# Optimization experiments

Hardware: AMD Instinct MI355X
Metric: run time of the kernel (lower is better)

The kernel has to match this reference:

```python
import jax, jax.numpy as jnp
import numpy as np

N_CB = 10          # n_codebooks
K = 2048           # codebook_size
D = 256            # codebook_dim
SEM = 256          # semantic_proj_dim
W2V = 1024         # w2v_bert_dim
COMMIT = 0.25      # commitment_cost


def setup_inputs() -> dict:
    key = jax.random.key(0)
    ks = jax.random.split(key, 7)
    B, T = 16, 1024
    z = jax.random.normal(ks[0], (B, T, D), jnp.float32)
    w2v_targets = jax.random.normal(ks[1], (B, T, W2V), jnp.float32)
    # codebooks: uniform(-1/K, 1/K) as in nn.init.uniform_
    E = jax.random.uniform(ks[2], (N_CB, K, D), jnp.float32, -1.0 / K, 1.0 / K)
    # semantic head: Linear(D, SEM) -> GELU -> Linear(SEM, W2V)
    W1 = jax.random.normal(ks[3], (D, SEM), jnp.float32) * (1.0 / np.sqrt(D))
    b1 = jnp.zeros((SEM,), jnp.float32)
    W2 = jax.random.normal(ks[4], (SEM, W2V), jnp.float32) * (1.0 / np.sqrt(SEM))
    b2 = jnp.zeros((W2V,), jnp.float32)
    return {"z": z, "w2v_targets": w2v_targets, "E": E,
            "W1": W1, "b1": b1, "W2": W2, "b2": b2}


def _vq_step(residual, Ei):
    """Single-codebook VQ with straight-through estimator.
    residual: (B,T,D); Ei: (K,D). Returns (z_q, indices, loss)."""
    sg = jax.lax.stop_gradient
    B, T, d = residual.shape
    flat = residual.reshape(-1, d)                      # (N, D)
    dist = (jnp.sum(flat * flat, axis=1, keepdims=True)
            - 2.0 * flat @ Ei.T
            + jnp.sum(Ei * Ei, axis=1))
    idx = jnp.argmin(dist, axis=1).reshape(B, T)        # (B, T)
    q = Ei[idx]                                         # (B, T, D) gather
    commitment_loss = jnp.mean((sg(q) - residual) ** 2)
    embedding_loss = jnp.mean((q - sg(residual)) ** 2)
    loss = embedding_loss + COMMIT * commitment_loss
    z_q = residual + sg(q - residual)                   # straight-through
    return z_q, idx, loss


def reference(z, w2v_targets, E, W1, b1, W2, b2):
    residual = z
    z_q_total = jnp.zeros_like(z)
    codes = []
    vq_loss = jnp.float32(0.0)
    semantic_loss = jnp.float32(0.0)
    for i in range(N_CB):
        z_q_i, idx_i, loss_i = _vq_step(residual, E[i])
        if i == 0:
            # semantic head on CB1 output (torch GELU default = exact erf)
            h = jax.nn.gelu(z_q_i @ W1 + b1, approximate=False)
            predicted = h @ W2 + b2                     # (B, T, W2V)
            semantic_loss = jnp.mean((predicted - w2v_targets) ** 2)
        z_q_total = z_q_total + z_q_i
        residual = residual - jax.lax.stop_gradient(z_q_i)
        vq_loss = vq_loss + loss_i
        codes.append(idx_i)
    all_codes = jnp.stack(codes, axis=-1)               # (B, T, N_CB)
    return z_q_total, all_codes, vq_loss, semantic_loss
```

## Files before the change

kernel.cpp:

```cpp
#include <hip/hip_runtime.h>
#include <float.h>
#include <math.h>

#define NTOK 16384
#define KCB  2048
#define DDIM 256
#define NCB  10
#define MARGIN 1.0e-3f

typedef __attribute__((ext_vector_type(8))) short  short8;
typedef __attribute__((ext_vector_type(4))) float  f32x4;

static __device__ __forceinline__ unsigned short f2bf(float f) {
    unsigned int b = __float_as_uint(f);
    unsigned int r = b + 0x7FFFu + ((b >> 16) & 1u);
    return (unsigned short)(r >> 16);
}
static __device__ __forceinline__ float bf2f(unsigned short h) {
    return __uint_as_float((unsigned int)h << 16);
}

__global__ __launch_bounds__(256) void norms_all_kernel(const float* __restrict__ E,
                                                        const float* __restrict__ z,
                                                        float* __restrict__ sseE,
                                                        float* __restrict__ normA) {
    const int gw   = (blockIdx.x * 256 + threadIdx.x) >> 6;
    const int lane = threadIdx.x & 63;
    const int row  = gw * 4 + (lane >> 4);
    const int l    = lane & 15;
    const float* src = nullptr; float* dst = nullptr;
    if (row < NCB * KCB)             { src = E + (size_t)row * DDIM;               dst = sseE + row; }
    else if (row < NCB * KCB + NTOK) { src = z + (size_t)(row - NCB * KCB) * DDIM; dst = normA + (row - NCB * KCB); }
    float r = 0.f;
    if (src) {
        const float* a = src + ((l >> 3) << 7) + (l & 7);
        float v = a[0];
        r = __fmul_rn(v, v);
        #pragma unroll
        for (int k = 1; k < 16; ++k) { v = a[k * 8]; r = __fadd_rn(r, __fmul_rn(v, v)); }
    }
    r = __fadd_rn(r, __shfl_xor(r, 1, 64));
    r = __fadd_rn(r, __shfl_xor(r, 2, 64));
    r = __fadd_rn(r, __shfl_xor(r, 4, 64));
    r = __fadd_rn(r, __shfl_xor(r, 8, 64));
    if (src && l == 0) *dst = r;
}

__global__ __launch_bounds__(256) void conv_all_kernel(const float* __restrict__ E,
                                                       const float* __restrict__ z,
                                                       const float* __restrict__ W1,
                                                       const float* __restrict__ W2,
                                                       unsigned short* __restrict__ Eh,
                                                       unsigned short* __restrict__ resH,
                                                       unsigned short* __restrict__ w1t,
                                                       unsigned short* __restrict__ w2t) {
    int i = blockIdx.x * 256 + threadIdx.x;
    if (i < 5242880) {
        Eh[i] = f2bf(E[i]);
    } else if (i < 9437184) {
        int j = i - 5242880;
        resH[j] = f2bf(z[j]);
    } else if (i < 9502720) {
        int j = i - 9437184;
        int n = j >> 8, k = j & 255;
        w1t[j] = f2bf(W1[k * 256 + n]);
    } else {
        int j = i - 9502720;
        int n = j >> 8, k = j & 255;
        w2t[j] = f2bf(W2[k * 1024 + n]);
    }
}

__global__ __launch_bounds__(256) void vq_screen(const unsigned short* __restrict__ resH,
                                                 const unsigned short* __restrict__ Ehi,
                                                 const float* __restrict__ sseEi,
                                                 int2* __restrict__ gSlots,
                                                 int* __restrict__ gCnt,
                                                 float* __restrict__ gMin) {
    __shared__ unsigned short sAh[128 * 40];
    __shared__ unsigned short sBh[128 * 40];
    __shared__ float sC[128];
    __shared__ int   lCnt[128];
    __shared__ int2  lSlot[128][4];
    const int tid = threadIdx.x;
    const int wv = tid >> 6, lane = tid & 63;
    const int l15 = lane & 15, qd = lane >> 4;
    const int tile = blockIdx.x >> 4, slice = blockIdx.x & 15;
    const int t0 = tile * 128, c0 = slice * 128;

    if (tid < 128) { lCnt[tid] = 0; sC[tid] = sseEi[c0 + tid]; }
    {
        int2 inf; inf.x = 0x7F800000; inf.y = 0;
        ((int2*)lSlot)[tid] = inf; ((int2*)lSlot)[tid + 256] = inf;
    }

    f32x4 acc[2][8];
    #pragma unroll
    for (int m = 0; m < 2; ++m)
        #pragma unroll
        for (int n = 0; n < 8; ++n) acc[m][n] = (f32x4){0.f, 0.f, 0.f, 0.f};

    const int r0 = tid >> 2, cc4 = tid & 3;
    const int r1 = (tid + 256) >> 2;
    for (int kc = 0; kc < 8; ++kc) {
        const int db = kc * 32;
        __syncthreads();
        *(uint4*)(sAh + r0 * 40 + cc4 * 8) = *(const uint4*)(resH + (size_t)(t0 + r0) * 256 + db + cc4 * 8);
        *(uint4*)(sAh + r1 * 40 + cc4 * 8) = *(const uint4*)(resH + (size_t)(t0 + r1) * 256 + db + cc4 * 8);
        *(uint4*)(sBh + r0 * 40 + cc4 * 8) = *(const uint4*)(Ehi  + (size_t)(c0 + r0) * 256 + db + cc4 * 8);
        *(uint4*)(sBh + r1 * 40 + cc4 * 8) = *(const uint4*)(Ehi  + (size_t)(c0 + r1) * 256 + db + cc4 * 8);
        __syncthreads();

        short8 ah[2];
        #pragma unroll
        for (int m = 0; m < 2; ++m)
            ah[m] = *(const short8*)(sAh + (wv * 32 + m * 16 + l15) * 40 + qd * 8);
        #pragma unroll
        for (int n = 0; n < 8; ++n) {
            short8 bh = *(const short8*)(sBh + (n * 16 + l15) * 40 + qd * 8);
            #pragma unroll
            for (int m = 0; m < 2; ++m)
                acc[m][n] = __builtin_amdgcn_mfma_f32_16x16x32_bf16(ah[m], bh, acc[m][n], 0, 0, 0);
        }
    }

    #pragma unroll
    for (int m = 0; m < 2; ++m)
        #pragma unroll
        for (int n = 0; n < 8; ++n) {
            float Cv = sC[n * 16 + l15];
            #pragma unroll
            for (int r = 0; r < 4; ++r) acc[m][n][r] = fmaf(-2.f, acc[m][n][r], Cv);
        }
    #pragma unroll
    for (int m = 0; m < 2; ++m)
        #pragma unroll
        for (int r = 0; r < 4; ++r) {
            float v = acc[m][0][r];
            #pragma unroll
            for (int n = 1; n < 8; ++n) v = fminf(v, acc[m][n][r]);
            v = fminf(v, __shfl_xor(v, 1, 64));
            v = fminf(v, __shfl_xor(v, 2, 64));
            v = fminf(v, __shfl_xor(v, 4, 64));
            v = fminf(v, __shfl_xor(v, 8, 64));
            int tloc = wv * 32 + m * 16 + qd * 4 + r;
            if (l15 == 0) gMin[(t0 + tloc) * 16 + slice] = v;
            float thr = v + MARGIN;
            #pragma unroll
            for (int n = 0; n < 8; ++n) {
                float sv = acc[m][n][r];
                if (sv <= thr) {
                    int pos = atomicAdd(&lCnt[tloc], 1);
                    if (pos < 4) {
                        int2 e; e.x = __float_as_int(sv); e.y = c0 + n * 16 + l15;
                        lSlot[tloc][pos] = e;
                    }
                }
            }
        }
    __syncthreads();
    {
        int tloc = tid >> 1, half = tid & 1;
        size_t base = (size_t)(t0 + tloc) * 64 + slice * 4 + half * 2;
        gSlots[base]     = lSlot[tloc][half * 2];
        gSlots[base + 1] = lSlot[tloc][half * 2 + 1];
        if (!half) gCnt[(t0 + tloc) * 16 + slice] = lCnt[tloc];
    }
}

static __device__ __forceinline__ float np_chain(const float* __restrict__ sRow,
                                                 const float* __restrict__ Ei,
                                                 int cc, float A, float C) {
    const float4* e = (const float4*)(Ei + (size_t)cc * DDIM);
    float a = 0.f;
    #pragma unroll 8
    for (int k = 0; k < 64; ++k) {
        float4 ev = e[k];
        const float4 rv = *(const float4*)(sRow + k * 4);
        a = fmaf(rv.x, ev.x, a); a = fmaf(rv.y, ev.y, a);
        a = fmaf(rv.z, ev.z, a); a = fmaf(rv.w, ev.w, a);
    }
    return __fadd_rn(fmaf(-2.f, a, A), C);
}

__global__ __launch_bounds__(256) void vq_post(const float* __restrict__ resSrc,
                                               const float* __restrict__ Ei,
                                               const float* __restrict__ sseEi,
                                               float* __restrict__ res,
                                               float* __restrict__ zq,
                                               float* __restrict__ codes,
                                               float* __restrict__ lossPart,
                                               float* __restrict__ normA,
                                               unsigned short* __restrict__ resHp,
                                               unsigned short* __restrict__ zqb,
                                               const int2* __restrict__ gSlots,
                                               const int* __restrict__ gCnt,
                                               const float* __restrict__ gMin,
                                               int iter) {
    __shared__ float sScr[4][4][256];
    const int tid = threadIdx.x;
    const int wv = tid >> 6, lane = tid & 63;
    const int g = lane >> 4, l15 = lane & 15;
    const int tb = blockIdx.x * 16 + wv * 4;
    float lsum = 0.f;

    int2 sl[4]; float4 r4[4]; int cnt4[4]; float smin4[4]; float4 zq4[4]; float A4[4];
    #pragma unroll
    for (int j = 0; j < 4; ++j) sl[j] = gSlots[(size_t)(tb + j) * 64 + lane];
    #pragma unroll
    for (int j = 0; j < 4; ++j)
        r4[j] = *(const float4*)(resSrc + (size_t)(tb + j) * DDIM + lane * 4);
    #pragma unroll
    for (int j = 0; j < 4; ++j) cnt4[j]  = (lane < 16) ? gCnt[(tb + j) * 16 + lane] : 0;
    #pragma unroll
    for (int j = 0; j < 4; ++j) smin4[j] = (lane < 16) ? gMin[(tb + j) * 16 + lane] : FLT_MAX;
    #pragma unroll
    for (int j = 0; j < 4; ++j) A4[j] = normA[tb + j];
    if (iter > 0) {
        #pragma unroll
        for (int j = 0; j < 4; ++j)
            zq4[j] = *(const float4*)(zq + (size_t)(tb + j) * DDIM + lane * 4);
    }

    int winner[4];
    #pragma unroll
    for (int j = 0; j < 4; ++j) {
        float gm = smin4[j];
        #pragma unroll
        for (int o = 32; o >= 1; o >>= 1) gm = fminf(gm, __shfl_xor(gm, o, 64));
        const float thr = gm + MARGIN;
        float sv = __int_as_float(sl[j].x);
        unsigned long long bal = __ballot((sv <= thr) ? 1 : 0);
        bool ovfRel = __any((lane < 16 && cnt4[j] > 4 && smin4[j] <= thr) ? 1 : 0);
        if (!ovfRel && __popcll(bal) == 1) {
            winner[j] = __shfl(sl[j].y, __ffsll(bal) - 1, 64);
        } else if (!ovfRel) {
            *(float4*)(&sScr[wv][j][lane * 4]) = r4[j];
            const bool qal = (sv <= thr);
            const int cc = qal ? sl[j].y : 0;
            float s = np_chain(sScr[wv][j], Ei, cc, A4[j], sseEi[cc]);
            unsigned long long best = qal
                ? (((unsigned long long)__float_as_uint(s) << 32) | (unsigned)cc)
                : ~0ULL;
            #pragma unroll
            for (int o = 32; o >= 1; o >>= 1) {
                unsigned long long ot = __shfl_xor(best, o, 64);
                if (ot < best) best = ot;
            }
            winner[j] = (int)(unsigned)(best & 0xFFFFFFFFu);
        } else {
            *(float4*)(&sScr[wv][j][lane * 4]) = r4[j];
            unsigned long long best = ~0ULL;
            for (int cc = lane; cc < KCB; cc += 64) {
                float s = np_chain(sScr[wv][j], Ei, cc, A4[j], sseEi[cc]);
                unsigned long long key =
                    ((unsigned long long)__float_as_uint(s) << 32) | (unsigned)cc;
                if (key < best) best = key;
            }
            #pragma unroll
            for (int o = 32; o >= 1; o >>= 1) {
                unsigned long long ot = __shfl_xor(best, o, 64);
                if (ot < best) best = ot;
            }
            winner[j] = (int)(unsigned)(best & 0xFFFFFFFFu);
        }
    }
    #pragma unroll
    for (int j = 0; j < 4; ++j)
        if (lane == j) codes[(size_t)(tb + j) * NCB + iter] = (float)winner[j];

    float4 q4[4];
    #pragma unroll
    for (int j = 0; j < 4; ++j)
        q4[j] = *(const float4*)(Ei + (size_t)winner[j] * DDIM + lane * 4);

    #pragma unroll
    for (int j = 0; j < 4; ++j) {
        const size_t go = (size_t)(tb + j) * DDIM + lane * 4;
        float4 rn4, zqi4;
        float tqx = q4[j].x - r4[j].x; zqi4.x = r4[j].x + tqx; rn4.x = r4[j].x - zqi4.x;
        float tqy = q4[j].y - r4[j].y; zqi4.y = r4[j].y + tqy; rn4.y = r4[j].y - zqi4.y;
        float tqz = q4[j].z - r4[j].z; zqi4.z = r4[j].z + tqz; rn4.z = r4[j].z - zqi4.z;
        float tqw = q4[j].w - r4[j].w; zqi4.w = r4[j].w + tqw; rn4.w = r4[j].w - zqi4.w;
        lsum = fmaf(tqx, tqx, lsum); lsum = fmaf(tqy, tqy, lsum);
        lsum = fmaf(tqz, tqz, lsum); lsum = fmaf(tqw, tqw, lsum);
        *(float4*)(res + go) = rn4;
        {
            unsigned short h[4] = { f2bf(rn4.x), f2bf(rn4.y), f2bf(rn4.z), f2bf(rn4.w) };
            *(ushort4*)(resHp + go) = *(ushort4*)h;
        }
        if (iter == 0) {
            *(float4*)(zq + go) = zqi4;
            unsigned short u[4] = { f2bf(zqi4.x), f2bf(zqi4.y), f2bf(zqi4.z), f2bf(zqi4.w) };
            *(ushort4*)(zqb + go) = *(ushort4*)u;
        } else {
            zq4[j].x += zqi4.x; zq4[j].y += zqi4.y;
            zq4[j].z += zqi4.z; zq4[j].w += zqi4.w;
            *(float4*)(zq + go) = zq4[j];
        }
        *(float4*)(&sScr[wv][j][lane * 4]) = rn4;
    }
    {
        const float* a = &sScr[wv][g][((l15 >> 3) << 7) + (l15 & 7)];
        float v = a[0];
        float r = __fmul_rn(v, v);
        #pragma unroll
        for (int k = 1; k < 16; ++k) { v = a[k * 8]; r = __fadd_rn(r, __fmul_rn(v, v)); }
        r = __fadd_rn(r, __shfl_xor(r, 1, 64));
        r = __fadd_rn(r, __shfl_xor(r, 2, 64));
        r = __fadd_rn(r, __shfl_xor(r, 4, 64));
        r = __fadd_rn(r, __shfl_xor(r, 8, 64));
        if (l15 == 0) normA[tb + g] = r;
    }
    #pragma unroll
    for (int o = 32; o >= 1; o >>= 1) lsum += __shfl_xor(lsum, o, 64);
    if (lane == 0) lossPart[iter * 4096 + blockIdx.x * 4 + wv] = lsum;
}

__global__ __launch_bounds__(256) void loss_final(const float* __restrict__ lossPart,
                                                  float* __restrict__ vql) {
    __shared__ float sRed[4];
    float s = 0.f;
    for (int i = threadIdx.x; i < 40960; i += 256) s += lossPart[i];
    #pragma unroll
    for (int o = 32; o >= 1; o >>= 1) s += __shfl_xor(s, o, 64);
    if ((threadIdx.x & 63) == 0) sRed[threadIdx.x >> 6] = s;
    __syncthreads();
    if (threadIdx.x == 0)
        vql[0] = (sRed[0] + sRed[1] + sRed[2] + sRed[3]) * (1.25f / 4194304.f);
}

__global__ __launch_bounds__(256) void semantic_mfma(const unsigned short* __restrict__ zqb,
                                                     const float* __restrict__ tgt,
                                                     const unsigned short* __restrict__ w1t,
                                                     const float* __restrict__ b1,
                                                     const unsigned short* __restrict__ w2t,
                                                     const float* __restrict__ b2,
                                                     float* __restrict__ semLoss) {
    __shared__ unsigned short sZ[32 * 264];
    __shared__ unsigned short sH[32 * 264];
    __shared__ float sRed[4];
    const int tid = threadIdx.x;
    const int wv = tid >> 6, lane = tid & 63;
    const int l15 = lane & 15, qd = lane >> 4;
    const int tb = blockIdx.x * 32;

    {
        int row = tid >> 3, seg = tid & 7;
        const uint4* src = (const uint4*)(zqb + (size_t)(tb + row) * 256);
        uint4* dst = (uint4*)(&sZ[row * 264]);
        #pragma unroll
        for (int p = 0; p < 4; ++p) dst[seg * 4 + p] = src[seg * 4 + p];
    }
    __syncthreads();

    short8 az[8][2];
    #pragma unroll
    for (int kc = 0; kc < 8; ++kc)
        #pragma unroll
        for (int m = 0; m < 2; ++m)
            az[kc][m] = *(const short8*)(&sZ[(16 * m + l15) * 264 + kc * 32 + qd * 8]);

    #pragma unroll
    for (int nt4 = 0; nt4 < 4; ++nt4) {
        const int nt = wv * 4 + nt4;
        f32x4 acc0 = {0.f,0.f,0.f,0.f}, acc1 = {0.f,0.f,0.f,0.f};
        const unsigned short* bb = w1t + (size_t)(16 * nt + l15) * 256 + qd * 8;
        #pragma unroll
        for (int kc = 0; kc < 8; ++kc) {
            short8 b = *(const short8*)(bb + kc * 32);
            acc0 = __builtin_amdgcn_mfma_f32_16x16x32_bf16(az[kc][0], b, acc0, 0, 0, 0);
            acc1 = __builtin_amdgcn_mfma_f32_16x16x32_bf16(az[kc][1], b, acc1, 0, 0, 0);
        }
        const float b1v = b1[16 * nt + l15];
        #pragma unroll
        for (int r = 0; r < 4; ++r) {
            float x0 = acc0[r] + b1v;
            float x1 = acc1[r] + b1v;
            sH[(4 * qd + r) * 264 + 16 * nt + l15]      = f2bf(0.5f * x0 * (1.f + erff(x0 * 0.70710678f)));
            sH[(16 + 4 * qd + r) * 264 + 16 * nt + l15] = f2bf(0.5f * x1 * (1.f + erff(x1 * 0.70710678f)));
        }
    }
    __syncthreads();

    short8 ah[8][2];
    #pragma unroll
    for (int kc = 0; kc < 8; ++kc)
        #pragma unroll
        for (int m = 0; m < 2; ++m)
            ah[kc][m] = *(const short8*)(&sH[(16 * m + l15) * 264 + kc * 32 + qd * 8]);

    float lsum = 0.f;
    for (int t = 0; t < 16; ++t) {
        const int nt = wv * 16 + t;
        f32x4 acc0 = {0.f,0.f,0.f,0.f}, acc1 = {0.f,0.f,0.f,0.f};
        const unsigned short* bb = w2t + (size_t)(16 * nt + l15) * 256 + qd * 8;
        #pragma unroll
        for (int kc = 0; kc < 8; ++kc) {
            short8 b = *(const short8*)(bb + kc * 32);
            acc0 = __builtin_amdgcn_mfma_f32_16x16x32_bf16(ah[kc][0], b, acc0, 0, 0, 0);
            acc1 = __builtin_amdgcn_mfma_f32_16x16x32_bf16(ah[kc][1], b, acc1, 0, 0, 0);
        }
        const int n = 16 * nt + l15;
        const float b2v = b2[n];
        #pragma unroll
        for (int r = 0; r < 4; ++r) {
            float dv0 = (acc0[r] + b2v) - tgt[(size_t)(tb + 4 * qd + r) * 1024 + n];
            float dv1 = (acc1[r] + b2v) - tgt[(size_t)(tb + 16 + 4 * qd + r) * 1024 + n];
            lsum = fmaf(dv0, dv0, lsum);
            lsum = fmaf(dv1, dv1, lsum);
        }
    }
    #pragma unroll
    for (int o = 32; o >= 1; o >>= 1) lsum += __shfl_xor(lsum, o, 64);
    if (lane == 0) sRed[wv] = lsum;
    __syncthreads();
    if (tid == 0)
        atomicAdd(semLoss, (sRed[0] + sRed[1] + sRed[2] + sRed[3]) * (1.0f / 16777216.f));
}

extern "C" void kernel_launch(void* const* d_in, const int* in_sizes, int n_in,
                              void* d_out, int out_size, void* d_ws, size_t ws_size,
                              hipStream_t stream) {
    const float* z   = (const float*)d_in[0];
    const float* tgt = (const float*)d_in[1];
    const float* E   = (const float*)d_in[2];
    const float* W1  = (const float*)d_in[3];
    const float* b1  = (const float*)d_in[4];
    const float* W2  = (const float*)d_in[5];
    const float* b2  = (const float*)d_in[6];

    float* out   = (float*)d_out;
    float* zq    = out;
    float* codes = out + (size_t)NTOK * DDIM;
    float* vql   = codes + (size_t)NTOK * NCB;

    char* w = (char*)d_ws;
    float*          res   = (float*)(w);
    unsigned short* resH  = (unsigned short*)(w + 16777216);
    unsigned short* Eh    = (unsigned short*)(w + 33554432);
    unsigned short* zqb   = (unsigned short*)(w + 54525952);
    int2*           gSlots= (int2*)(w + 62914560);
    int*            gCnt  = (int*)(w + 71303168);
    float*          gMin  = (float*)(w + 72351744);
    float*          sseE  = (float*)(w + 73400320);
    float*          normA = (float*)(w + 73531392);
    float*          lossPart=(float*)(w + 73662464);
    unsigned short* w1t   = (unsigned short*)(w + 73924608);
    unsigned short* w2t   = (unsigned short*)(w + 74055680);

    hipMemsetAsync(vql, 0, 2 * sizeof(float), stream);
    norms_all_kernel<<<9216, 256, 0, stream>>>(E, z, sseE, normA);
    conv_all_kernel<<<38144, 256, 0, stream>>>(E, z, W1, W2, Eh, resH, w1t, w2t);
    for (int it = 0; it < NCB; ++it) {
        const float*          Ei    = E  + (size_t)it * KCB * DDIM;
        const unsigned short* Ehi   = Eh + (size_t)it * KCB * DDIM;
        const float*          sseEi = sseE + (size_t)it * KCB;
        const float* resSrc = (it == 0) ? z : res;
        vq_screen<<<2048, 256, 0, stream>>>(resH, Ehi, sseEi, gSlots, gCnt, gMin);
        vq_post<<<1024, 256, 0, stream>>>(resSrc, Ei, sseEi, res, zq, codes, lossPart,
                                          normA, resH, zqb, gSlots, gCnt, gMin, it);
        if (it == 0)
            semantic_mfma<<<512, 256, 0, stream>>>(zqb, tgt, w1t, b1, w2t, b2, vql + 1);
    }
    loss_final<<<1, 256, 0, stream>>>(lossPart, vql);
}
```

Before: 1.103 ms.

## Fuse semantic head into second screen launch and merge prep kernels

Merges the norms and bf16 conversion kernels into one prep launch. Removes the standalone semantic-head launch and folds its blocks into the iteration-1 screen kernel, interleaving one semantic block per four screen blocks and sharing LDS through a union, so the semantic GEMMs overlap with the codebook screening. It also halves the vq_post block size to 128 threads with twice as many blocks, and prefetches targets in the semantic loop. The costs are a larger LDS footprint for the fused kernel, possible load imbalance between heterogeneous blocks, and scheduling changes from the resized post kernel.

```diff
diff --git a/kernel.cpp b/kernel.cpp
--- a/kernel.cpp
+++ b/kernel.cpp
@@ -20,78 +20,86 @@
     return __uint_as_float((unsigned int)h << 16);
 }
 
-__global__ __launch_bounds__(256) void norms_all_kernel(const float* __restrict__ E,
-                                                        const float* __restrict__ z,
-                                                        float* __restrict__ sseE,
-                                                        float* __restrict__ normA) {
-    const int gw   = (blockIdx.x * 256 + threadIdx.x) >> 6;
-    const int lane = threadIdx.x & 63;
-    const int row  = gw * 4 + (lane >> 4);
-    const int l    = lane & 15;
-    const float* src = nullptr; float* dst = nullptr;
-    if (row < NCB * KCB)             { src = E + (size_t)row * DDIM;               dst = sseE + row; }
-    else if (row < NCB * KCB + NTOK) { src = z + (size_t)(row - NCB * KCB) * DDIM; dst = normA + (row - NCB * KCB); }
-    float r = 0.f;
-    if (src) {
-        const float* a = src + ((l >> 3) << 7) + (l & 7);
-        float v = a[0];
-        r = __fmul_rn(v, v);
-        #pragma unroll
-        for (int k = 1; k < 16; ++k) { v = a[k * 8]; r = __fadd_rn(r, __fmul_rn(v, v)); }
-    }
-    r = __fadd_rn(r, __shfl_xor(r, 1, 64));
-    r = __fadd_rn(r, __shfl_xor(r, 2, 64));
-    r = __fadd_rn(r, __shfl_xor(r, 4, 64));
-    r = __fadd_rn(r, __shfl_xor(r, 8, 64));
-    if (src && l == 0) *dst = r;
-}
-
-__global__ __launch_bounds__(256) void conv_all_kernel(const float* __restrict__ E,
-                                                       const float* __restrict__ z,
-                                                       const float* __restrict__ W1,
-                                                       const float* __restrict__ W2,
-                                                       unsigned short* __restrict__ Eh,
-                                                       unsigned short* __restrict__ resH,
-                                                       unsigned short* __restrict__ w1t,
-                                                       unsigned short* __restrict__ w2t) {
-    int i = blockIdx.x * 256 + threadIdx.x;
-    if (i < 5242880) {
-        Eh[i] = f2bf(E[i]);
-    } else if (i < 9437184) {
-        int j = i - 5242880;
-        resH[j] = f2bf(z[j]);
-    } else if (i < 9502720) {
-        int j = i - 9437184;
-        int n = j >> 8, k = j & 255;
-        w1t[j] = f2bf(W1[k * 256 + n]);
+__global__ __launch_bounds__(256) void prep_all(const float* __restrict__ E,
+                                                const float* __restrict__ z,
+                                                const float* __restrict__ W1,
+                                                const float* __restrict__ W2,
+                                                float* __restrict__ sseE,
+                                                float* __restrict__ normA,
+                                                unsigned short* __restrict__ Eh,
+                                                unsigned short* __restrict__ resH,
+                                                unsigned short* __restrict__ w1t,
+                                                unsigned short* __restrict__ w2t) {
+    if (blockIdx.x < 38144) {
+        int i = blockIdx.x * 256 + threadIdx.x;
+        if (i < 5242880) {
+            Eh[i] = f2bf(E[i]);
+        } else if (i < 9437184) {
+            int j = i - 5242880;
+            resH[j] = f2bf(z[j]);
+        } else if (i < 9502720) {
+            int j = i - 9437184;
+            int n = j >> 8, k = j & 255;
+            w1t[j] = f2bf(W1[k * 256 + n]);
+        } else {
+            int j = i - 9502720;
+            int n = j >> 8, k = j & 255;
+            w2t[j] = f2bf(W2[k * 1024 + n]);
+        }
     } else {
-        int j = i - 9502720;
-        int n = j >> 8, k = j & 255;
-        w2t[j] = f2bf(W2[k * 1024 + n]);
-    }
-}
-
-__global__ __launch_bounds__(256) void vq_screen(const unsigned short* __restrict__ resH,
-                                                 const unsigned short* __restrict__ Ehi,
-                                                 const float* __restrict__ sseEi,
-                                                 int2* __restrict__ gSlots,
-                                                 int* __restrict__ gCnt,
-                                                 float* __restrict__ gMin) {
-    __shared__ unsigned short sAh[128 * 40];
-    __shared__ unsigned short sBh[128 * 40];
-    __shared__ float sC[128];
-    __shared__ int   lCnt[128];
-    __shared__ int2  lSlot[128][4];
+        const int gw   = ((blockIdx.x - 38144) * 256 + threadIdx.x) >> 6;
+        const int lane = threadIdx.x & 63;
+        const int row  = gw * 4 + (lane >> 4);
+        const int l    = lane & 15;
+        const float* src = nullptr; float* dst = nullptr;
+        if (row < NCB * KCB)             { src = E + (size_t)row * DDIM;               dst = sseE + row; }
+        else if (row < NCB * KCB + NTOK) { src = z + (size_t)(row - NCB * KCB) * DDIM; dst = normA + (row - NCB * KCB); }
+        float r = 0.f;
+        if (src) {
+            const float* a = src + ((l >> 3) << 7) + (l & 7);
+            float v = a[0];
+            r = __fmul_rn(v, v);
+            #pragma unroll
+            for (int k = 1; k < 16; ++k) { v = a[k * 8]; r = __fadd_rn(r, __fmul_rn(v, v)); }
+        }
+        r = __fadd_rn(r, __shfl_xor(r, 1, 64));
+        r = __fadd_rn(r, __shfl_xor(r, 2, 64));
+        r = __fadd_rn(r, __shfl_xor(r, 4, 64));
+        r = __fadd_rn(r, __shfl_xor(r, 8, 64));
+        if (src && l == 0) *dst = r;
+    }
+}
+
+struct ScrLds {
+    unsigned short sAh[128 * 40];
+    unsigned short sBh[128 * 40];
+    float sC[128];
+    int   lCnt[128];
+    int2  lSlot[128][4];
+};
+struct SemLds {
+    unsigned short sZ[32 * 264];
+    float sRed[4];
+};
+union FusedLds { ScrLds scr; SemLds sem; };
+
+static __device__ __forceinline__ void screen_body(const int scrIdx, ScrLds& L,
+                                                   const unsigned short* __restrict__ resH,
+                                                   const unsigned short* __restrict__ Ehi,
+                                                   const float* __restrict__ sseEi,
+                                                   int2* __restrict__ gSlots,
+                                                   int* __restrict__ gCnt,
+                                                   float* __restrict__ gMin) {
     const int tid = threadIdx.x;
     const int wv = tid >> 6, lane = tid & 63;
     const int l15 = lane & 15, qd = lane >> 4;
-    const int tile = blockIdx.x >> 4, slice = blockIdx.x & 15;
+    const int tile = scrIdx >> 4, slice = scrIdx & 15;
     const int t0 = tile * 128, c0 = slice * 128;
 
-    if (tid < 128) { lCnt[tid] = 0; sC[tid] = sseEi[c0 + tid]; }
+    if (tid < 128) { L.lCnt[tid] = 0; L.sC[tid] = sseEi[c0 + tid]; }
     {
         int2 inf; inf.x = 0x7F800000; inf.y = 0;
-        ((int2*)lSlot)[tid] = inf; ((int2*)lSlot)[tid + 256] = inf;
+        ((int2*)L.lSlot)[tid] = inf; ((int2*)L.lSlot)[tid + 256] = inf;
     }
 
     f32x4 acc[2][8];
@@ -105,19 +113,19 @@
     for (int kc = 0; kc < 8; ++kc) {
         const int db = kc * 32;
         __syncthreads();
-        *(uint4*)(sAh + r0 * 40 + cc4 * 8) = *(const uint4*)(resH + (size_t)(t0 + r0) * 256 + db + cc4 * 8);
-        *(uint4*)(sAh + r1 * 40 + cc4 * 8) = *(const uint4*)(resH + (size_t)(t0 + r1) * 256 + db + cc4 * 8);
-        *(uint4*)(sBh + r0 * 40 + cc4 * 8) = *(const uint4*)(Ehi  + (size_t)(c0 + r0) * 256 + db + cc4 * 8);
-        *(uint4*)(sBh + r1 * 40 + cc4 * 8) = *(const uint4*)(Ehi  + (size_t)(c0 + r1) * 256 + db + cc4 * 8);
+        *(uint4*)(L.sAh + r0 * 40 + cc4 * 8) = *(const uint4*)(resH + (size_t)(t0 + r0) * 256 + db + cc4 * 8);
+        *(uint4*)(L.sAh + r1 * 40 + cc4 * 8) = *(const uint4*)(resH + (size_t)(t0 + r1) * 256 + db + cc4 * 8);
+        *(uint4*)(L.sBh + r0 * 40 + cc4 * 8) = *(const uint4*)(Ehi  + (size_t)(c0 + r0) * 256 + db + cc4 * 8);
+        *(uint4*)(L.sBh + r1 * 40 + cc4 * 8) = *(const uint4*)(Ehi  + (size_t)(c0 + r1) * 256 + db + cc4 * 8);
         __syncthreads();
 
         short8 ah[2];
         #pragma unroll
         for (int m = 0; m < 2; ++m)
-            ah[m] = *(const short8*)(sAh + (wv * 32 + m * 16 + l15) * 40 + qd * 8);
+            ah[m] = *(const short8*)(L.sAh + (wv * 32 + m * 16 + l15) * 40 + qd * 8);
         #pragma unroll
         for (int n = 0; n < 8; ++n) {
-            short8 bh = *(const short8*)(sBh + (n * 16 + l15) * 40 + qd * 8);
+            short8 bh = *(const short8*)(L.sBh + (n * 16 + l15) * 40 + qd * 8);
             #pragma unroll
             for (int m = 0; m < 2; ++m)
                 acc[m][n] = __builtin_amdgcn_mfma_f32_16x16x32_bf16(ah[m], bh, acc[m][n], 0, 0, 0);
@@ -128,7 +136,7 @@
     for (int m = 0; m < 2; ++m)
         #pragma unroll
         for (int n = 0; n < 8; ++n) {
-            float Cv = sC[n * 16 + l15];
+            float Cv = L.sC[n * 16 + l15];
             #pragma unroll
             for (int r = 0; r < 4; ++r) acc[m][n][r] = fmaf(-2.f, acc[m][n][r], Cv);
         }
@@ -150,10 +158,10 @@
             for (int n = 0; n < 8; ++n) {
                 float sv = acc[m][n][r];
                 if (sv <= thr) {
-                    int pos = atomicAdd(&lCnt[tloc], 1);
+                    int pos = atomicAdd(&L.lCnt[tloc], 1);
                     if (pos < 4) {
                         int2 e; e.x = __float_as_int(sv); e.y = c0 + n * 16 + l15;
-                        lSlot[tloc][pos] = e;
+                        L.lSlot[tloc][pos] = e;
                     }
                 }
             }
@@ -162,10 +170,137 @@
     {
         int tloc = tid >> 1, half = tid & 1;
         size_t base = (size_t)(t0 + tloc) * 64 + slice * 4 + half * 2;
-        gSlots[base]     = lSlot[tloc][half * 2];
-        gSlots[base + 1] = lSlot[tloc][half * 2 + 1];
-        if (!half) gCnt[(t0 + tloc) * 16 + slice] = lCnt[tloc];
-    }
+        gSlots[base]     = L.lSlot[tloc][half * 2];
+        gSlots[base + 1] = L.lSlot[tloc][half * 2 + 1];
+        if (!half) gCnt[(t0 + tloc) * 16 + slice] = L.lCnt[tloc];
+    }
+}
+
+static __device__ __forceinline__ void semantic_body(const int semIdx, SemLds& L,
+                                                     const unsigned short* __restrict__ zqb,
+                                                     const float* __restrict__ tgt,
+                                                     const unsigned short* __restrict__ w1t,
+                                                     const float* __restrict__ b1,
+                                                     const unsigned short* __restrict__ w2t,
+                                                     const float* __restrict__ b2,
+                                                     float* __restrict__ semLoss) {
+    const int tid = threadIdx.x;
+    const int wv = tid >> 6, lane = tid & 63;
+    const int l15 = lane & 15, qd = lane >> 4;
+    const int tb = semIdx * 32;
+    unsigned short* sH = L.sZ;
+
+    {
+        int row = tid >> 3, seg = tid & 7;
+        const uint4* src = (const uint4*)(zqb + (size_t)(tb + row) * 256);
+        uint4* dst = (uint4*)(&L.sZ[row * 264]);
+        #pragma unroll
+        for (int p = 0; p < 4; ++p) dst[seg * 4 + p] = src[seg * 4 + p];
+    }
+    __syncthreads();
+
+    short8 az[8][2];
+    #pragma unroll
+    for (int kc = 0; kc < 8; ++kc)
+        #pragma unroll
+        for (int m = 0; m < 2; ++m)
+            az[kc][m] = *(const short8*)(&L.sZ[(16 * m + l15) * 264 + kc * 32 + qd * 8]);
+    __syncthreads();
+
+    #pragma unroll
+    for (int nt4 = 0; nt4 < 4; ++nt4) {
+        const int nt = wv * 4 + nt4;
+        f32x4 acc0 = {0.f,0.f,0.f,0.f}, acc1 = {0.f,0.f,0.f,0.f};
+        const unsigned short* bb = w1t + (size_t)(16 * nt + l15) * 256 + qd * 8;
+        #pragma unroll
+        for (int kc = 0; kc < 8; ++kc) {
+            short8 b = *(const short8*)(bb + kc * 32);
+            acc0 = __builtin_amdgcn_mfma_f32_16x16x32_bf16(az[kc][0], b, acc0, 0, 0, 0);
+            acc1 = __builtin_amdgcn_mfma_f32_16x16x32_bf16(az[kc][1], b, acc1, 0, 0, 0);
+        }
+        const float b1v = b1[16 * nt + l15];
+        #pragma unroll
+        for (int r = 0; r < 4; ++r) {
+            float x0 = acc0[r] + b1v;
+            float x1 = acc1[r] + b1v;
+            sH[(4 * qd + r) * 264 + 16 * nt + l15]      = f2bf(0.5f * x0 * (1.f + erff(x0 * 0.70710678f)));
+            sH[(16 + 4 * qd + r) * 264 + 16 * nt + l15] = f2bf(0.5f * x1 * (1.f + erff(x1 * 0.70710678f)));
+        }
+    }
+    __syncthreads();
+
+    short8 ah[8][2];
+    #pragma unroll
+    for (int kc = 0; kc < 8; ++kc)
+        #pragma unroll
+        for (int m = 0; m < 2; ++m)
+            ah[kc][m] = *(const short8*)(&sH[(16 * m + l15) * 264 + kc * 32 + qd * 8]);
+
+    float lsum = 0.f;
+    #pragma unroll 2
+    for (int t = 0; t < 16; ++t) {
+        const int nt = wv * 16 + t;
+        const int n = 16 * nt + l15;
+        float tg0[4], tg1[4];
+        #pragma unroll
+        for (int r = 0; r < 4; ++r) {
+            tg0[r] = tgt[(size_t)(tb + 4 * qd + r) * 1024 + n];
+            tg1[r] = tgt[(size_t)(tb + 16 + 4 * qd + r) * 1024 + n];
+        }
+        f32x4 acc0 = {0.f,0.f,0.f,0.f}, acc1 = {0.f,0.f,0.f,0.f};
+        const unsigned short* bb = w2t + (size_t)(16 * nt + l15) * 256 + qd * 8;
+        #pragma unroll
+        for (int kc = 0; kc < 8; ++kc) {
+            short8 b = *(const short8*)(bb + kc * 32);
+            acc0 = __builtin_amdgcn_mfma_f32_16x16x32_bf16(ah[kc][0], b, acc0, 0, 0, 0);
+            acc1 = __builtin_amdgcn_mfma_f32_16x16x32_bf16(ah[kc][1], b, acc1, 0, 0, 0);
+        }
+        const float b2v = b2[n];
+        #pragma unroll
+        for (int r = 0; r < 4; ++r) {
+            float dv0 = (acc0[r] + b2v) - tg0[r];
+            float dv1 = (acc1[r] + b2v) - tg1[r];
+            lsum = fmaf(dv0, dv0, lsum);
+            lsum = fmaf(dv1, dv1, lsum);
+        }
+    }
+    #pragma unroll
+    for (int o = 32; o >= 1; o >>= 1) lsum += __shfl_xor(lsum, o, 64);
+    if (lane == 0) L.sRed[wv] = lsum;
+    __syncthreads();
+    if (tid == 0)
+        atomicAdd(semLoss, (L.sRed[0] + L.sRed[1] + L.sRed[2] + L.sRed[3]) * (1.0f / 16777216.f));
+}
+
+__global__ __launch_bounds__(256) void vq_screen(const unsigned short* __restrict__ resH,
+                                                 const unsigned short* __restrict__ Ehi,
+                                                 const float* __restrict__ sseEi,
+                                                 int2* __restrict__ gSlots,
+                                                 int* __restrict__ gCnt,
+                                                 float* __restrict__ gMin) {
+    __shared__ ScrLds L;
+    screen_body(blockIdx.x, L, resH, Ehi, sseEi, gSlots, gCnt, gMin);
+}
+
+__global__ __launch_bounds__(256) void screen_sem(const unsigned short* __restrict__ resH,
+                                                  const unsigned short* __restrict__ Ehi,
+                                                  const float* __restrict__ sseEi,
+                                                  int2* __restrict__ gSlots,
+                                                  int* __restrict__ gCnt,
+                                                  float* __restrict__ gMin,
+                                                  const unsigned short* __restrict__ zqb,
+                                                  const float* __restrict__ tgt,
+                                                  const unsigned short* __restrict__ w1t,
+                                                  const float* __restrict__ b1,
+                                                  const unsigned short* __restrict__ w2t,
+                                                  const float* __restrict__ b2,
+                                                  float* __restrict__ semLoss) {
+    __shared__ FusedLds U;
+    const int b = blockIdx.x, grp = b / 5, rem = b % 5;
+    if (rem == 4)
+        semantic_body(grp, U.sem, zqb, tgt, w1t, b1, w2t, b2, semLoss);
+    else
+        screen_body(grp * 4 + rem, U.scr, resH, Ehi, sseEi, gSlots, gCnt, gMin);
 }
 
 static __device__ __forceinline__ float np_chain(const float* __restrict__ sRow,
@@ -183,7 +318,7 @@
     return __fadd_rn(fmaf(-2.f, a, A), C);
 }
 
-__global__ __launch_bounds__(256) void vq_post(const float* __restrict__ resSrc,
+__global__ __launch_bounds__(128) void vq_post(const float* __restrict__ resSrc,
                                                const float* __restrict__ Ei,
                                                const float* __restrict__ sseEi,
                                                float* __restrict__ res,
@@ -197,11 +332,11 @@
                                                const int* __restrict__ gCnt,
                                                const float* __restrict__ gMin,
                                                int iter) {
-    __shared__ float sScr[4][4][256];
+    __shared__ float sScr[2][4][256];
     const int tid = threadIdx.x;
     const int wv = tid >> 6, lane = tid & 63;
     const int g = lane >> 4, l15 = lane & 15;
-    const int tb = blockIdx.x * 16 + wv * 4;
+    const int tb = blockIdx.x * 8 + wv * 4;
     float lsum = 0.f;
 
     int2 sl[4]; float4 r4[4]; int cnt4[4]; float smin4[4]; float4 zq4[4]; float A4[4];
@@ -314,7 +449,7 @@
     }
     #pragma unroll
     for (int o = 32; o >= 1; o >>= 1) lsum += __shfl_xor(lsum, o, 64);
-    if (lane == 0) lossPart[iter * 4096 + blockIdx.x * 4 + wv] = lsum;
+    if (lane == 0) lossPart[iter * 4096 + blockIdx.x * 2 + wv] = lsum;
 }
 
 __global__ __launch_bounds__(256) void loss_final(const float* __restrict__ lossPart,
@@ -328,95 +463,6 @@
     __syncthreads();
     if (threadIdx.x == 0)
         vql[0] = (sRed[0] + sRed[1] + sRed[2] + sRed[3]) * (1.25f / 4194304.f);
-}
-
-__global__ __launch_bounds__(256) void semantic_mfma(const unsigned short* __restrict__ zqb,
-                                                     const float* __restrict__ tgt,
-                                                     const unsigned short* __restrict__ w1t,
-                                                     const float* __restrict__ b1,
-                                                     const unsigned short* __restrict__ w2t,
-                                                     const float* __restrict__ b2,
-                                                     float* __restrict__ semLoss) {
-    __shared__ unsigned short sZ[32 * 264];
-    __shared__ unsigned short sH[32 * 264];
-    __shared__ float sRed[4];
-    const int tid = threadIdx.x;
-    const int wv = tid >> 6, lane = tid & 63;
-    const int l15 = lane & 15, qd = lane >> 4;
-    const int tb = blockIdx.x * 32;
-
-    {
-        int row = tid >> 3, seg = tid & 7;
-        const uint4* src = (const uint4*)(zqb + (size_t)(tb + row) * 256);
-        uint4* dst = (uint4*)(&sZ[row * 264]);
-        #pragma unroll
-        for (int p = 0; p < 4; ++p) dst[seg * 4 + p] = src[seg * 4 + p];
-    }
-    __syncthreads();
-
-    short8 az[8][2];
-    #pragma unroll
-    for (int kc = 0; kc < 8; ++kc)
-        #pragma unroll
-        for (int m = 0; m < 2; ++m)
-            az[kc][m] = *(const short8*)(&sZ[(16 * m + l15) * 264 + kc * 32 + qd * 8]);
-
-    #pragma unroll
-    for (int nt4 = 0; nt4 < 4; ++nt4) {
-        const int nt = wv * 4 + nt4;
-        f32x4 acc0 = {0.f,0.f,0.f,0.f}, acc1 = {0.f,0.f,0.f,0.f};
-        const unsigned short* bb = w1t + (size_t)(16 * nt + l15) * 256 + qd * 8;
-        #pragma unroll
-        for (int kc = 0; kc < 8; ++kc) {
-            short8 b = *(const short8*)(bb + kc * 32);
-            acc0 = __builtin_amdgcn_mfma_f32_16x16x32_bf16(az[kc][0], b, acc0, 0, 0, 0);
-            acc1 = __builtin_amdgcn_mfma_f32_16x16x32_bf16(az[kc][1], b, acc1, 0, 0, 0);
-        }
-        const float b1v = b1[16 * nt + l15];
-        #pragma unroll
-        for (int r = 0; r < 4; ++r) {
-            float x0 = acc0[r] + b1v;
-            float x1 = acc1[r] + b1v;
-            sH[(4 * qd + r) * 264 + 16 * nt + l15]      = f2bf(0.5f * x0 * (1.f + erff(x0 * 0.70710678f)));
-            sH[(16 + 4 * qd + r) * 264 + 16 * nt + l15] = f2bf(0.5f * x1 * (1.f + erff(x1 * 0.70710678f)));
-        }
-    }
-    __syncthreads();
-
-    short8 ah[8][2];
-    #pragma unroll
-    for (int kc = 0; kc < 8; ++kc)
-        #pragma unroll
-        for (int m = 0; m < 2; ++m)
-            ah[kc][m] = *(const short8*)(&sH[(16 * m + l15) * 264 + kc * 32 + qd * 8]);
-
-    float lsum = 0.f;
-    for (int t = 0; t < 16; ++t) {
-        const int nt = wv * 16 + t;
-        f32x4 acc0 = {0.f,0.f,0.f,0.f}, acc1 = {0.f,0.f,0.f,0.f};
-        const unsigned short* bb = w2t + (size_t)(16 * nt + l15) * 256 + qd * 8;
-        #pragma unroll
-        for (int kc = 0; kc < 8; ++kc) {
-            short8 b = *(const short8*)(bb + kc * 32);
-            acc0 = __builtin_amdgcn_mfma_f32_16x16x32_bf16(ah[kc][0], b, acc0, 0, 0, 0);
-            acc1 = __builtin_amdgcn_mfma_f32_16x16x32_bf16(ah[kc][1], b, acc1, 0, 0, 0);
-        }
-        const int n = 16 * nt + l15;
-        const float b2v = b2[n];
-        #pragma unroll
-        for (int r = 0; r < 4; ++r) {
-            float dv0 = (acc0[r] + b2v) - tgt[(size_t)(tb + 4 * qd + r) * 1024 + n];
-            float dv1 = (acc1[r] + b2v) - tgt[(size_t)(tb + 16 + 4 * qd + r) * 1024 + n];
-            lsum = fmaf(dv0, dv0, lsum);
-            lsum = fmaf(dv1, dv1, lsum);
-        }
-    }
-    #pragma unroll
-    for (int o = 32; o >= 1; o >>= 1) lsum += __shfl_xor(lsum, o, 64);
-    if (lane == 0) sRed[wv] = lsum;
-    __syncthreads();
-    if (tid == 0)
-        atomicAdd(semLoss, (sRed[0] + sRed[1] + sRed[2] + sRed[3]) * (1.0f / 16777216.f));
 }
 
 extern "C" void kernel_launch(void* const* d_in, const int* in_sizes, int n_in,
@@ -450,18 +496,19 @@
     unsigned short* w2t   = (unsigned short*)(w + 74055680);
 
     hipMemsetAsync(vql, 0, 2 * sizeof(float), stream);
-    norms_all_kernel<<<9216, 256, 0, stream>>>(E, z, sseE, normA);
-    conv_all_kernel<<<38144, 256, 0, stream>>>(E, z, W1, W2, Eh, resH, w1t, w2t);
+    prep_all<<<47360, 256, 0, stream>>>(E, z, W1, W2, sseE, normA, Eh, resH, w1t, w2t);
     for (int it = 0; it < NCB; ++it) {
         const float*          Ei    = E  + (size_t)it * KCB * DDIM;
         const unsigned short* Ehi   = Eh + (size_t)it * KCB * DDIM;
         const float*          sseEi = sseE + (size_t)it * KCB;
         const float* resSrc = (it == 0) ? z : res;
-        vq_screen<<<2048, 256, 0, stream>>>(resH, Ehi, sseEi, gSlots, gCnt, gMin);
-        vq_post<<<1024, 256, 0, stream>>>(resSrc, Ei, sseEi, res, zq, codes, lossPart,
+        if (it == 1)
+            screen_sem<<<2560, 256, 0, stream>>>(resH, Ehi, sseEi, gSlots, gCnt, gMin,
+                                                 zqb, tgt, w1t, b1, w2t, b2, vql + 1);
+        else
+            vq_screen<<<2048, 256, 0, stream>>>(resH, Ehi, sseEi, gSlots, gCnt, gMin);
+        vq_post<<<2048, 128, 0, stream>>>(resSrc, Ei, sseEi, res, zq, codes, lossPart,
                                           normA, resH, zqb, gSlots, gCnt, gMin, it);
-        if (it == 0)
-            semantic_mfma<<<512, 256, 0, stream>>>(zqb, tgt, w1t, b1, w2t, b2, vql + 1);
     }
     loss_final<<<1, 256, 0, stream>>>(lossPart, vql);
 }
```

After: 1.142 ms. 3.5% more time.
